# Kernel tuning notes

Measured on AMD Instinct MI355X. Metric: run time of the kernel, lower is better.

## Reference

```python
import jax, jax.numpy as jnp
import numpy as np

B, T, S, E, H, D = 4, 1024, 1024, 1024, 16, 64


def _ln(x, g, b, eps=1e-5):
    m = x.mean(-1, keepdims=True)
    v = ((x - m) ** 2).mean(-1, keepdims=True)
    return (x - m) * jax.lax.rsqrt(v + eps) * g + b


def _mha(xq, xkv, mask4, Wq, Wk, Wv, Wo, bo):
    # Wq/Wk/Wv: [H, E, D] (stacked per-head bias-free linears)
    q = jnp.einsum('bte,hed->bhtd', xq, Wq)
    k = jnp.einsum('bse,hed->bhsd', xkv, Wk)
    v = jnp.einsum('bse,hed->bhsd', xkv, Wv)
    # NOTE: original scales by C**-0.5 with C = n_embd, not head_size
    wei = jnp.einsum('bhtd,bhsd->bhts', q, k) * (float(E) ** -0.5)
    wei = jnp.where(mask4 == 0, jnp.float32(-1e9), wei)
    wei = jax.nn.softmax(wei, axis=-1)
    o = jnp.einsum('bhts,bhsd->bhtd', wei, v)  # [B,H,T,D]
    b_, h_, t_, d_ = o.shape
    o = o.transpose(0, 2, 1, 3).reshape(b_, t_, h_ * d_)
    return o @ Wo + bo


def setup_inputs() -> dict:
    key = jax.random.key(0)
    ks = jax.random.split(key, 24)
    sd = 0.02
    inp = {
        'x': jax.random.normal(ks[0], (B, T, E), jnp.float32),
        'x_m': jnp.ones((B, 1, T), jnp.int32),
        'ca': jax.random.normal(ks[1], (B, S, E), jnp.float32),
        'ca_m': jnp.ones((B, 1, S), jnp.int32),
        'Wq_s': jax.random.normal(ks[2], (H, E, D), jnp.float32) * sd,
        'Wk_s': jax.random.normal(ks[3], (H, E, D), jnp.float32) * sd,
        'Wv_s': jax.random.normal(ks[4], (H, E, D), jnp.float32) * sd,
        'Wo_s': jax.random.normal(ks[5], (E, E), jnp.float32) * sd,
        'bo_s': jnp.zeros((E,), jnp.float32),
        'Wq_c': jax.random.normal(ks[6], (H, E, D), jnp.float32) * sd,
        'Wk_c': jax.random.normal(ks[7], (H, E, D), jnp.float32) * sd,
        'Wv_c': jax.random.normal(ks[8], (H, E, D), jnp.float32) * sd,
        'Wo_c': jax.random.normal(ks[9], (E, E), jnp.float32) * sd,
        'bo_c': jnp.zeros((E,), jnp.float32),
        'ln1_g': jnp.ones((E,), jnp.float32), 'ln1_b': jnp.zeros((E,), jnp.float32),
        'ln2_g': jnp.ones((E,), jnp.float32), 'ln2_b': jnp.zeros((E,), jnp.float32),
        'ln3_g': jnp.ones((E,), jnp.float32), 'ln3_b': jnp.zeros((E,), jnp.float32),
        'W1': jax.random.normal(ks[10], (E, 4 * E), jnp.float32) * sd,
        'b1': jnp.zeros((4 * E,), jnp.float32),
        'W2': jax.random.normal(ks[11], (4 * E, E), jnp.float32) * sd,
        'b2': jnp.zeros((E,), jnp.float32),
    }
    return inp


def reference(x, x_m, ca, ca_m, Wq_s, Wk_s, Wv_s, Wo_s, bo_s,
              Wq_c, Wk_c, Wv_c, Wo_c, bo_c,
              ln1_g, ln1_b, ln2_g, ln2_b, ln3_g, ln3_b,
              W1, b1, W2, b2):
    tril = jnp.tril(jnp.ones((T, T), jnp.int32))
    # self-attn mask: x_m [B,1,T] & tril [T,T] -> [B,1,T,T] (broadcast over heads)
    self_mask = x_m[:, :, None, :] * tril          # [B,1,T,T]
    cross_mask = ca_m[:, :, None, :]               # [B,1,1,S]
    x = x + _mha(_ln(x, ln1_g, ln1_b), _ln(x, ln1_g, ln1_b) if False else _ln(x, ln1_g, ln1_b), self_mask, Wq_s, Wk_s, Wv_s, Wo_s, bo_s)
    x = x + _mha(_ln(x, ln2_g, ln2_b), ca, cross_mask, Wq_c, Wk_c, Wv_c, Wo_c, bo_c)
    h = _ln(x, ln3_g, ln3_b)
    x = x + (jax.nn.relu(h @ W1 + b1) @ W2 + b2)
    return x
```

## Files before the change

kernel.cpp:

```cpp
#include <hip/hip_runtime.h>
#include <hip/hip_bf16.h>
#include <cstdint>
#include <cstddef>

typedef __attribute__((ext_vector_type(8))) short  s8v;
typedef __attribute__((ext_vector_type(4))) short  s4v;
typedef __attribute__((ext_vector_type(8))) __bf16 b8v;
typedef __attribute__((ext_vector_type(4))) float  f32x4;
typedef __attribute__((ext_vector_type(4))) unsigned u32x4;

__device__ __forceinline__ short f2bf(float f){
  unsigned u = __builtin_bit_cast(unsigned, f);
  unsigned r = (u + 0x7fffu + ((u >> 16) & 1u)) >> 16;
  return (short)(unsigned short)r;
}

__device__ __forceinline__ f32x4 mfma16(s8v a, s8v b, f32x4 c){
  return __builtin_amdgcn_mfma_f32_16x16x32_bf16(
      __builtin_bit_cast(b8v, a), __builtin_bit_cast(b8v, b), c, 0, 0, 0);
}

__device__ __forceinline__ unsigned cvtpk(float a, float b){
  unsigned w;
  asm("v_cvt_pk_bf16_f32 %0, %1, %2" : "=v"(w) : "v"(a), "v"(b));
  return w;
}

__global__ __launch_bounds__(256)
void ln_k(const float* __restrict__ x, const float* __restrict__ g,
          const float* __restrict__ b, short* __restrict__ out)
{
  const int row = blockIdx.x, tid = threadIdx.x;
  const float4 v = ((const float4*)(x + (size_t)row*1024))[tid];
  float s  = v.x+v.y+v.z+v.w;
  float s2 = v.x*v.x+v.y*v.y+v.z*v.z+v.w*v.w;
  #pragma unroll
  for (int off=32; off; off>>=1){ s += __shfl_down(s, off); s2 += __shfl_down(s2, off); }
  __shared__ float red[8];
  const int wave = tid>>6, lane = tid&63;
  if (lane==0){ red[wave]=s; red[4+wave]=s2; }
  __syncthreads();
  s  = red[0]+red[1]+red[2]+red[3];
  s2 = red[4]+red[5]+red[6]+red[7];
  const float mean = s*(1.f/1024.f);
  const float rstd = rsqrtf(s2*(1.f/1024.f) - mean*mean + 1e-5f);
  const float4 gv = ((const float4*)g)[tid];
  const float4 bv = ((const float4*)b)[tid];
  s4v o;
  o[0] = f2bf((v.x-mean)*rstd*gv.x + bv.x);
  o[1] = f2bf((v.y-mean)*rstd*gv.y + bv.y);
  o[2] = f2bf((v.z-mean)*rstd*gv.z + bv.z);
  o[3] = f2bf((v.w-mean)*rstd*gv.w + bv.w);
  *(s4v*)(out + (size_t)row*1024 + tid*4) = o;
}

__global__ __launch_bounds__(256)
void cast_k(const float* __restrict__ in, short* __restrict__ out)
{
  const int i = blockIdx.x*256 + threadIdx.x;
  const float4 v = ((const float4*)in)[i];
  s4v o; o[0]=f2bf(v.x); o[1]=f2bf(v.y); o[2]=f2bf(v.z); o[3]=f2bf(v.w);
  ((s4v*)out)[i] = o;
}

__global__ __launch_bounds__(256)
void tcast_k(const float* __restrict__ in, short* __restrict__ out, int E2, int D2)
{
  __shared__ float t[32][33];
  const int h  = blockIdx.z;
  const int e0 = blockIdx.x*32, d0 = blockIdx.y*32;
  const int tx = threadIdx.x & 31, ty = threadIdx.x >> 5;
  const float* ip = in + (size_t)h*E2*D2;
  #pragma unroll
  for (int r = ty; r < 32; r += 8)
    t[r][tx] = ip[(size_t)(e0+r)*D2 + d0 + tx];
  __syncthreads();
  short* op = out + (size_t)h*D2*E2;
  #pragma unroll
  for (int r = ty; r < 32; r += 8)
    op[(size_t)(d0+r)*E2 + e0 + tx] = f2bf(t[tx][r]);
}

__global__ __launch_bounds__(256)
void vtrans_k(const short* __restrict__ V, int ldv, short* __restrict__ Vt, int S, int H)
{
  __shared__ short t[32][34];
  const int bh = blockIdx.z;
  const int b = bh / H, h = bh % H;
  const int s0 = blockIdx.x*32, d0 = blockIdx.y*32;
  const int tx = threadIdx.x & 31, ty = threadIdx.x >> 5;
  const short* ip = V + (size_t)b*S*ldv + h*64;
  #pragma unroll
  for (int r = ty; r < 32; r += 8)
    t[r][tx] = ip[(size_t)(s0+r)*ldv + d0 + tx];
  __syncthreads();
  short* op = Vt + ((size_t)bh*64 + d0)*S + s0;
  #pragma unroll
  for (int r = ty; r < 32; r += 8)
    op[(size_t)r*S + tx] = t[tx][r];
}

template<int BN, int BIAS, int RELU, int RESID, int WF32>
__global__ __launch_bounds__(256, 2)
void gemm_bt(const short* __restrict__ A, const short* __restrict__ Bt,
             const float* __restrict__ bias, const float* __restrict__ resid,
             short* __restrict__ Cb, float* __restrict__ Cf,
             int M, int N, int K)
{
  __shared__ short lds[3][128*32 + BN*32];
  const int nwg = gridDim.x * gridDim.y;
  int id = blockIdx.y * gridDim.x + blockIdx.x;
  id = (id & 7) * (nwg >> 3) + (id >> 3);
  const int bx = id % gridDim.x, by = id / gridDim.x;
  const int m0 = by*128, n0 = bx*BN;

  const int tid  = threadIdx.x;
  const int wave = tid>>6, lane = tid&63;
  const int lo = lane&15, hi = lane>>4;
  const int wm = wave>>1, wn = wave&1;

  constexpr int NJ = BN/32;
  constexpr int BC = BN>>6;
  f32x4 acc[4][NJ] = {};
  const int NK = K >> 5;

  auto stage = [&](int buf, int kt){
    const short* Ag = A  + (size_t)m0*K + kt*32;
    const short* Bg = Bt + (size_t)n0*K + kt*32;
    #pragma unroll
    for (int c=0;c<2;c++){
      const int q = (wave*2+c)*64 + lane;
      const int r = q>>2, cc = q&3;
      __builtin_amdgcn_global_load_lds(
        (const __attribute__((address_space(1))) void*)(Ag + (size_t)r*K + cc*8),
        (__attribute__((address_space(3))) void*)(&lds[buf][(wave*2+c)*512]),
        16, 0, 0);
    }
    #pragma unroll
    for (int c=0;c<BC;c++){
      const int q = (wave*BC+c)*64 + lane;
      const int r = q>>2, cc = q&3;
      __builtin_amdgcn_global_load_lds(
        (const __attribute__((address_space(1))) void*)(Bg + (size_t)r*K + cc*8),
        (__attribute__((address_space(3))) void*)(&lds[buf][4096 + (wave*BC+c)*512]),
        16, 0, 0);
    }
  };

  stage(0, 0);
  if (NK > 1) stage(1, 1);

  for (int kt=0; kt<NK; kt++){
    if (kt+1 < NK){
      if constexpr (BN==128) asm volatile("s_waitcnt vmcnt(4)" ::: "memory");
      else                   asm volatile("s_waitcnt vmcnt(3)" ::: "memory");
    } else {
      asm volatile("s_waitcnt vmcnt(0)" ::: "memory");
    }
    __builtin_amdgcn_s_barrier();
    __builtin_amdgcn_sched_barrier(0);
    if (kt+2 < NK) stage((kt+2)%3, kt+2);

    const short* la = &lds[kt%3][0];
    const short* lb = &lds[kt%3][4096];
    s8v af[4], bfr[NJ];
    #pragma unroll
    for (int i=0;i<4;i++)
      af[i] = *(const s8v*)(la + (wm*64 + i*16 + lo)*32 + hi*8);
    #pragma unroll
    for (int j=0;j<NJ;j++)
      bfr[j] = *(const s8v*)(lb + (wn*(BN/2) + j*16 + lo)*32 + hi*8);
    #pragma unroll
    for (int i=0;i<4;i++)
      #pragma unroll
      for (int j=0;j<NJ;j++)
        acc[i][j] = mfma16(af[i], bfr[j], acc[i][j]);
  }

  #pragma unroll
  for (int i=0;i<4;i++){
    const int row = m0 + wm*64 + i*16 + hi*4;
    #pragma unroll
    for (int j=0;j<NJ;j++){
      const int col = n0 + wn*(BN/2) + j*16 + lo;
      const float bv = BIAS ? bias[col] : 0.0f;
      #pragma unroll
      for (int r=0;r<4;r++){
        float v = acc[i][j][r] + bv;
        if (RELU) v = fmaxf(v, 0.0f);
        const size_t idx = (size_t)(row + r)*N + col;
        if (RESID) v += resid[idx];
        if (WF32) Cf[idx] = v; else Cb[idx] = f2bf(v);
      }
    }
  }
}

template<int CAUSAL>
__global__ __launch_bounds__(256, 4)
void attn_k(const short* __restrict__ Q, int ldq,
            const short* __restrict__ K, int ldk,
            const short* __restrict__ Vt, int ldvt,
            const int* __restrict__ msk,
            short* __restrict__ O, int ldo,
            int H, int Tq, int Sk)
{
  __shared__ short kls[2][4096];
  __shared__ short vls[2][4096];
  const int bh = blockIdx.x;
  const int b = bh / H, h = bh % H;
  const int tid = threadIdx.x;
  const int wave = tid>>6, lane = tid&63;
  const int lo = lane&15, hi = lane>>4;
  const int t0 = blockIdx.y*64 + wave*16;

  const short* Qb  = Q + (size_t)(b*Tq)*ldq + h*64;
  const short* Kb  = K + (size_t)(b*Sk)*ldk + h*64;
  const short* Vtb = Vt + (size_t)bh*64*ldvt;
  const int*   mb  = msk + (size_t)b*Sk;

  const short* qp = Qb + (size_t)(t0+lo)*ldq + hi*8;
  const s8v qa0 = *(const s8v*)(qp);
  const s8v qa1 = *(const s8v*)(qp + 32);

  float mrow = -INFINITY, lrow = 0.f;
  f32x4 oacc[4] = {};
  const int trow = t0 + lo;
  const int nblk = CAUSAL ? (blockIdx.y + 1) : (Sk>>6);
  const float sc2 = 0.03125f * 1.44269504088896f;
  const int x8 = lo & 7;

  auto stage = [&](int buf, int it){
    const int s0 = it*64;
    #pragma unroll
    for (int rd=0; rd<2; rd++){
      const int q = rd*256 + tid;
      const int r = q>>3, c = q&7;
      const int cs = (c ^ (r&7))*8;
      __builtin_amdgcn_global_load_lds(
        (const __attribute__((address_space(1))) void*)(Kb + (size_t)(s0+r)*ldk + cs),
        (__attribute__((address_space(3))) void*)(&kls[buf][(rd*256 + wave*64)*8]),
        16, 0, 0);
      __builtin_amdgcn_global_load_lds(
        (const __attribute__((address_space(1))) void*)(Vtb + (size_t)r*ldvt + s0 + cs),
        (__attribute__((address_space(3))) void*)(&vls[buf][(rd*256 + wave*64)*8]),
        16, 0, 0);
    }
  };

  stage(0, 0);
  int cur = 0;
  for (int it=0; it<nblk; it++){
    __syncthreads();
    if (it+1 < nblk) stage(cur^1, it+1);
    const int s0 = it*64;

    int ka[4][4];
    #pragma unroll
    for (int g=0; g<4; g++){
      const int4 kv = ((const int4*)mb)[(s0>>2) + g*4 + hi];
      ka[g][0]=kv.x; ka[g][1]=kv.y; ka[g][2]=kv.z; ka[g][3]=kv.w;
    }

    const short* kl = kls[cur];
    s8v kf[4][2];
    #pragma unroll
    for (int g=0; g<4; g++){
      const int rb = (g*16 + lo)*64;
      kf[g][0] = *(const s8v*)(kl + rb + ((hi     ^ x8)*8));
      kf[g][1] = *(const s8v*)(kl + rb + (((4+hi) ^ x8)*8));
    }

    f32x4 sg[4] = {};
    __builtin_amdgcn_s_setprio(1);
    #pragma unroll
    for (int g=0; g<4; g++){
      sg[g] = mfma16(kf[g][0], qa0, sg[g]);
      sg[g] = mfma16(kf[g][1], qa1, sg[g]);
    }
    __builtin_amdgcn_s_setprio(0);

    const bool lastblk = CAUSAL && (it == nblk-1);
    float p[4][4];
    #pragma unroll
    for (int g=0; g<4; g++)
      #pragma unroll
      for (int r=0; r<4; r++){
        const int sidx = s0 + g*16 + 4*hi + r;
        const bool ok = ka[g][r] && (!lastblk || sidx <= trow);
        p[g][r] = ok ? sg[g][r]*sc2 : -1.5e9f;
      }

    float bmax;
    {
      float m0_ = fmaxf(fmaxf(p[0][0],p[0][1]), fmaxf(p[0][2],p[0][3]));
      float m1_ = fmaxf(fmaxf(p[1][0],p[1][1]), fmaxf(p[1][2],p[1][3]));
      float m2_ = fmaxf(fmaxf(p[2][0],p[2][1]), fmaxf(p[2][2],p[2][3]));
      float m3_ = fmaxf(fmaxf(p[3][0],p[3][1]), fmaxf(p[3][2],p[3][3]));
      bmax = fmaxf(fmaxf(m0_,m1_), fmaxf(m2_,m3_));
    }
    bmax = fmaxf(bmax, __shfl_xor(bmax, 16));
    bmax = fmaxf(bmax, __shfl_xor(bmax, 32));

    const float mn  = fmaxf(mrow, bmax);
    const float fac = exp2f(mrow - mn);
    mrow = mn;
    #pragma unroll
    for (int g=0; g<4; g++)
      #pragma unroll
      for (int r=0; r<4; r++)
        p[g][r] = exp2f(p[g][r] - mn);

    float bsum;
    {
      float s0_ = (p[0][0]+p[0][1]) + (p[0][2]+p[0][3]);
      float s1_ = (p[1][0]+p[1][1]) + (p[1][2]+p[1][3]);
      float s2_ = (p[2][0]+p[2][1]) + (p[2][2]+p[2][3]);
      float s3_ = (p[3][0]+p[3][1]) + (p[3][2]+p[3][3]);
      bsum = (s0_+s1_) + (s2_+s3_);
    }
    bsum += __shfl_xor(bsum, 16);
    bsum += __shfl_xor(bsum, 32);
    lrow = lrow*fac + bsum;
    #pragma unroll
    for (int f=0; f<4; f++)
      #pragma unroll
      for (int r=0; r<4; r++)
        oacc[f][r] *= fac;

    u32x4 pw0, pw1;
    pw0[0] = cvtpk(p[0][0], p[0][1]);
    pw0[1] = cvtpk(p[0][2], p[0][3]);
    pw0[2] = cvtpk(p[1][0], p[1][1]);
    pw0[3] = cvtpk(p[1][2], p[1][3]);
    pw1[0] = cvtpk(p[2][0], p[2][1]);
    pw1[1] = cvtpk(p[2][2], p[2][3]);
    pw1[2] = cvtpk(p[3][0], p[3][1]);
    pw1[3] = cvtpk(p[3][2], p[3][3]);
    const s8v pb0 = __builtin_bit_cast(s8v, pw0);
    const s8v pb1 = __builtin_bit_cast(s8v, pw1);

    const short* vl = vls[cur];
    __builtin_amdgcn_s_setprio(1);
    #pragma unroll
    for (int f=0; f<4; f++){
      const int rb = (f*16 + lo)*64;
      const int h2 = hi>>1, o2 = (hi&1)*4;
      const s4v a0 = *(const s4v*)(vl + rb + (((h2  ) ^ x8)*8) + o2);
      const s4v a1 = *(const s4v*)(vl + rb + (((2+h2) ^ x8)*8) + o2);
      const s4v a2 = *(const s4v*)(vl + rb + (((4+h2) ^ x8)*8) + o2);
      const s4v a3 = *(const s4v*)(vl + rb + (((6+h2) ^ x8)*8) + o2);
      const s8v av0 = __builtin_shufflevector(a0, a1, 0,1,2,3,4,5,6,7);
      const s8v av1 = __builtin_shufflevector(a2, a3, 0,1,2,3,4,5,6,7);
      oacc[f] = mfma16(av0, pb0, oacc[f]);
      oacc[f] = mfma16(av1, pb1, oacc[f]);
    }
    __builtin_amdgcn_s_setprio(0);
    cur ^= 1;
  }

  const float inv = 1.0f / lrow;
  short* Ob = O + (size_t)(b*Tq)*ldo + h*64 + (size_t)(t0+lo)*ldo + 4*hi;
  #pragma unroll
  for (int f=0; f<4; f++){
    s4v o;
    #pragma unroll
    for (int r=0; r<4; r++) o[r] = f2bf(oacc[f][r]*inv);
    *(s4v*)(Ob + f*16) = o;
  }
}

extern "C" void kernel_launch(void* const* d_in, const int* in_sizes, int n_in,
                              void* d_out, int out_size, void* d_ws, size_t ws_size,
                              hipStream_t stream)
{
  (void)in_sizes; (void)n_in; (void)out_size; (void)ws_size;
  const float* x    = (const float*)d_in[0];
  const int*   xm   = (const int*)  d_in[1];
  const float* ca   = (const float*)d_in[2];
  const int*   cam  = (const int*)  d_in[3];
  const float* Wq_s = (const float*)d_in[4];
  const float* Wk_s = (const float*)d_in[5];
  const float* Wv_s = (const float*)d_in[6];
  const float* Wo_s = (const float*)d_in[7];
  const float* bo_s = (const float*)d_in[8];
  const float* Wq_c = (const float*)d_in[9];
  const float* Wk_c = (const float*)d_in[10];
  const float* Wv_c = (const float*)d_in[11];
  const float* Wo_c = (const float*)d_in[12];
  const float* bo_c = (const float*)d_in[13];
  const float* ln1g = (const float*)d_in[14];
  const float* ln1b = (const float*)d_in[15];
  const float* ln2g = (const float*)d_in[16];
  const float* ln2b = (const float*)d_in[17];
  const float* ln3g = (const float*)d_in[18];
  const float* ln3b = (const float*)d_in[19];
  const float* W1   = (const float*)d_in[20];
  const float* b1   = (const float*)d_in[21];
  const float* W2   = (const float*)d_in[22];
  const float* b2   = (const float*)d_in[23];
  float* out = (float*)d_out;

  char* ws = (char*)d_ws;
  size_t off = 0;
  auto alloc = [&](size_t bytes)->void*{
    void* p = ws + off; off += (bytes + 255) & ~(size_t)255; return p; };

  short* w_qkv_s = (short*)alloc((size_t)3072*1024*2);
  short* w_o_s   = (short*)alloc((size_t)1024*1024*2);
  short* w_q_c   = (short*)alloc((size_t)1024*1024*2);
  short* w_kv_c  = (short*)alloc((size_t)2048*1024*2);
  short* w_o_c   = (short*)alloc((size_t)1024*1024*2);
  short* w_1     = (short*)alloc((size_t)4096*1024*2);
  short* w_2     = (short*)alloc((size_t)1024*4096*2);
  short* xn      = (short*)alloc((size_t)4096*1024*2);
  short* cab     = (short*)alloc((size_t)4096*1024*2);
  short* qkv     = (short*)alloc((size_t)4096*3072*2);
  short* attno   = (short*)alloc((size_t)4096*1024*2);
  float* xres    = (float*)alloc((size_t)4096*1024*4);
  short* hffn    = (short*)alloc((size_t)4096*4096*2);
  short* kvbuf   = qkv + (size_t)4096*1024;
  short* vt_s    = hffn;
  short* vt_c    = hffn + (size_t)4*1024*1024;

  tcast_k<<<dim3(32,  2,16),256,0,stream>>>(Wq_s, w_qkv_s,           1024,   64);
  tcast_k<<<dim3(32,  2,16),256,0,stream>>>(Wk_s, w_qkv_s+1024*1024, 1024,   64);
  tcast_k<<<dim3(32,  2,16),256,0,stream>>>(Wv_s, w_qkv_s+2048*1024, 1024,   64);
  tcast_k<<<dim3(32, 32, 1),256,0,stream>>>(Wo_s, w_o_s,             1024, 1024);
  tcast_k<<<dim3(32,  2,16),256,0,stream>>>(Wq_c, w_q_c,             1024,   64);
  tcast_k<<<dim3(32,  2,16),256,0,stream>>>(Wk_c, w_kv_c,            1024,   64);
  tcast_k<<<dim3(32,  2,16),256,0,stream>>>(Wv_c, w_kv_c+1024*1024,  1024,   64);
  tcast_k<<<dim3(32, 32, 1),256,0,stream>>>(Wo_c, w_o_c,             1024, 1024);
  tcast_k<<<dim3(32,128, 1),256,0,stream>>>(W1,   w_1,               1024, 4096);
  tcast_k<<<dim3(128,32, 1),256,0,stream>>>(W2,   w_2,               4096, 1024);
  cast_k<<<4096,256,0,stream>>>(ca, cab);

  ln_k<<<4096,256,0,stream>>>(x, ln1g, ln1b, xn);
  gemm_bt<128,0,0,0,0><<<dim3(24,32),256,0,stream>>>(xn, w_qkv_s, nullptr, nullptr,
                                                     qkv, nullptr, 4096, 3072, 1024);
  vtrans_k<<<dim3(32,2,64),256,0,stream>>>(qkv+2048, 3072, vt_s, 1024, 16);
  attn_k<1><<<dim3(64,16),256,0,stream>>>(qkv, 3072, qkv+1024, 3072, vt_s, 1024,
                                          xm, attno, 1024, 16, 1024, 1024);
  gemm_bt<64,1,0,1,1><<<dim3(16,32),256,0,stream>>>(attno, w_o_s, bo_s, x,
                                                    nullptr, xres, 4096, 1024, 1024);

  ln_k<<<4096,256,0,stream>>>(xres, ln2g, ln2b, xn);
  gemm_bt<64,0,0,0,0><<<dim3(16,32),256,0,stream>>>(xn, w_q_c, nullptr, nullptr,
                                                    qkv, nullptr, 4096, 1024, 1024);
  gemm_bt<64,0,0,0,0><<<dim3(32,32),256,0,stream>>>(cab, w_kv_c, nullptr, nullptr,
                                                    kvbuf, nullptr, 4096, 2048, 1024);
  vtrans_k<<<dim3(32,2,64),256,0,stream>>>(kvbuf+1024, 2048, vt_c, 1024, 16);
  attn_k<0><<<dim3(64,16),256,0,stream>>>(qkv, 1024, kvbuf, 2048, vt_c, 1024,
                                          cam, attno, 1024, 16, 1024, 1024);
  gemm_bt<64,1,0,1,1><<<dim3(16,32),256,0,stream>>>(attno, w_o_c, bo_c, xres,
                                                    nullptr, xres, 4096, 1024, 1024);

  ln_k<<<4096,256,0,stream>>>(xres, ln3g, ln3b, xn);
  gemm_bt<128,1,1,0,0><<<dim3(32,32),256,0,stream>>>(xn, w_1, b1, nullptr,
                                                     hffn, nullptr, 4096, 4096, 1024);
  gemm_bt<64,1,0,1,1><<<dim3(16,32),256,0,stream>>>(hffn, w_2, b2, xres,
                                                    nullptr, out, 4096, 1024, 4096);
}
```

Measured before the change: 394.3 us.

## Add 256x128 eight-wave GEMM with swizzled LDS and split-K FFN down-projection

Adds a new 512-thread GEMM kernel with 256x128 output tiles, 64-wide K steps, XOR-swizzled LDS staging through direct global-to-LDS loads, a three-buffer prefetch pipeline and raised wave priority around the MFMA blocks. It replaces the self-attention QKV, cross-attention KV and FFN up-projection GEMMs. The FFN down-projection is split into two K-halves writing fp32 partial sums, and a separate reduction kernel adds them together with bias and residual. The intent is more data reuse per tile and more blocks for the down-projection. The cost is extra partial-sum memory traffic, one more kernel launch, and occupancy limited to one block per CU.

```diff
diff --git a/kernel.cpp b/kernel.cpp
--- a/kernel.cpp
+++ b/kernel.cpp
@@ -100,6 +100,22 @@
     op[(size_t)r*S + tx] = t[tx][r];
 }
 
+__global__ __launch_bounds__(256)
+void red2_k(const float* __restrict__ pa, const float* __restrict__ pb,
+            const float* __restrict__ bias, const float* __restrict__ resid,
+            float* __restrict__ out, int N)
+{
+  const int i = blockIdx.x*256 + threadIdx.x;
+  const float4 va = ((const float4*)pa)[i];
+  const float4 vb = ((const float4*)pb)[i];
+  const float4 vr = ((const float4*)resid)[i];
+  const float4 bv = ((const float4*)bias)[i & (N/4 - 1)];
+  float4 o;
+  o.x = va.x+vb.x+bv.x+vr.x; o.y = va.y+vb.y+bv.y+vr.y;
+  o.z = va.z+vb.z+bv.z+vr.z; o.w = va.w+vb.w+bv.w+vr.w;
+  ((float4*)out)[i] = o;
+}
+
 template<int BN, int BIAS, int RELU, int RESID, int WF32>
 __global__ __launch_bounds__(256, 2)
 void gemm_bt(const short* __restrict__ A, const short* __restrict__ Bt,
@@ -187,6 +203,117 @@
       #pragma unroll
       for (int r=0;r<4;r++){
         float v = acc[i][j][r] + bv;
+        if (RELU) v = fmaxf(v, 0.0f);
+        const size_t idx = (size_t)(row + r)*N + col;
+        if (RESID) v += resid[idx];
+        if (WF32) Cf[idx] = v; else Cb[idx] = f2bf(v);
+      }
+    }
+  }
+}
+
+template<int BIAS, int RELU, int RESID, int WF32>
+__global__ __launch_bounds__(512, 1)
+void gemm8(const short* __restrict__ A, int lda,
+           const short* __restrict__ Bt, int ldb,
+           const float* __restrict__ bias, const float* __restrict__ resid,
+           short* __restrict__ Cb, float* __restrict__ Cf,
+           int M, int N, int K)
+{
+  __shared__ short lds[3][24576];
+  const int nwg = gridDim.x * gridDim.y;
+  int id = blockIdx.y * gridDim.x + blockIdx.x;
+  id = (id & 7) * (nwg >> 3) + (id >> 3);
+  const int bx = id % gridDim.x, by = id / gridDim.x;
+  const int m0 = by*256, n0 = bx*128;
+
+  const int tid = threadIdx.x;
+  const int lane = tid&63, wave = tid>>6;
+  const int lo = lane&15, hi = lane>>4;
+  const int wr = wave>>2, wc = wave&3;
+  const int x8 = lo&7;
+
+  f32x4 acc[8][2] = {};
+  const int NT = K >> 6;
+
+  auto stageA = [&](int buf, int kt, int part){
+    const short* Ag = A + (size_t)m0*lda + kt*64;
+    #pragma unroll
+    for (int j=0;j<2;j++){
+      const int q = (part*2+j)*512 + tid;
+      const int r = q>>3, c = q&7;
+      __builtin_amdgcn_global_load_lds(
+        (const __attribute__((address_space(1))) void*)(Ag + (size_t)r*lda + ((c^(r&7))*8)),
+        (__attribute__((address_space(3))) void*)(&lds[buf][q*8]), 16, 0, 0);
+    }
+  };
+  auto stageB = [&](int buf, int kt, int part){
+    const short* Bg = Bt + (size_t)n0*ldb + kt*64;
+    const int q = part*512 + tid;
+    const int r = q>>3, c = q&7;
+    __builtin_amdgcn_global_load_lds(
+      (const __attribute__((address_space(1))) void*)(Bg + (size_t)r*ldb + ((c^(r&7))*8)),
+      (__attribute__((address_space(3))) void*)(&lds[buf][16384 + q*8]), 16, 0, 0);
+  };
+
+  stageA(0,0,0); stageA(0,0,1); stageB(0,0,0); stageB(0,0,1);
+  if (NT>1){ stageA(1,1,0); stageA(1,1,1); stageB(1,1,0); stageB(1,1,1); }
+  asm volatile("s_waitcnt vmcnt(6)" ::: "memory");
+  __builtin_amdgcn_s_barrier();
+
+  for (int t=0; t<NT; t++){
+    const short* la = &lds[t%3][0];
+    const short* lb = &lds[t%3][16384];
+    const int nb = (t+2)%3;
+    const bool pf = (t+2 < NT);
+    #pragma unroll
+    for (int q=0; q<4; q++){
+      const int mh = q>>1, ks = q&1;
+      s8v af[4], bf2[2];
+      #pragma unroll
+      for (int i=0;i<4;i++){
+        const int row = wr*128 + (mh*4+i)*16 + lo;
+        af[i] = *(const s8v*)(la + row*64 + (((ks*4+hi)^x8)*8));
+      }
+      #pragma unroll
+      for (int j=0;j<2;j++){
+        const int row = wc*32 + j*16 + lo;
+        bf2[j] = *(const s8v*)(lb + row*64 + (((ks*4+hi)^x8)*8));
+      }
+      if (pf){
+        if      (q==0) stageA(nb, t+2, 0);
+        else if (q==1) stageA(nb, t+2, 1);
+        else if (q==2) stageB(nb, t+2, 0);
+        else           stageB(nb, t+2, 1);
+      }
+      __builtin_amdgcn_s_barrier();
+      asm volatile("s_waitcnt lgkmcnt(0)" ::: "memory");
+      __builtin_amdgcn_sched_barrier(0);
+      __builtin_amdgcn_s_setprio(1);
+      #pragma unroll
+      for (int i=0;i<4;i++)
+        #pragma unroll
+        for (int j=0;j<2;j++)
+          acc[mh*4+i][j] = mfma16(af[i], bf2[j], acc[mh*4+i][j]);
+      __builtin_amdgcn_s_setprio(0);
+      if (q==3 && t+1 < NT){
+        if (pf) asm volatile("s_waitcnt vmcnt(6)" ::: "memory");
+        else    asm volatile("s_waitcnt vmcnt(0)" ::: "memory");
+      }
+      __builtin_amdgcn_s_barrier();
+    }
+  }
+
+  #pragma unroll
+  for (int I=0;I<8;I++){
+    const int row = m0 + wr*128 + I*16 + hi*4;
+    #pragma unroll
+    for (int j=0;j<2;j++){
+      const int col = n0 + wc*32 + j*16 + lo;
+      const float bv = BIAS ? bias[col] : 0.0f;
+      #pragma unroll
+      for (int r=0;r<4;r++){
+        float v = acc[I][j][r] + bv;
         if (RELU) v = fmaxf(v, 0.0f);
         const size_t idx = (size_t)(row + r)*N + col;
         if (RESID) v += resid[idx];
@@ -419,6 +546,8 @@
   short* attno   = (short*)alloc((size_t)4096*1024*2);
   float* xres    = (float*)alloc((size_t)4096*1024*4);
   short* hffn    = (short*)alloc((size_t)4096*4096*2);
+  float* pA      = (float*)alloc((size_t)4096*1024*4);
+  float* pB      = (float*)alloc((size_t)4096*1024*4);
   short* kvbuf   = qkv + (size_t)4096*1024;
   short* vt_s    = hffn;
   short* vt_c    = hffn + (size_t)4*1024*1024;
@@ -436,8 +565,9 @@
   cast_k<<<4096,256,0,stream>>>(ca, cab);
 
   ln_k<<<4096,256,0,stream>>>(x, ln1g, ln1b, xn);
-  gemm_bt<128,0,0,0,0><<<dim3(24,32),256,0,stream>>>(xn, w_qkv_s, nullptr, nullptr,
-                                                     qkv, nullptr, 4096, 3072, 1024);
+  gemm8<0,0,0,0><<<dim3(24,16),512,0,stream>>>(xn, 1024, w_qkv_s, 1024,
+                                               nullptr, nullptr, qkv, nullptr,
+                                               4096, 3072, 1024);
   vtrans_k<<<dim3(32,2,64),256,0,stream>>>(qkv+2048, 3072, vt_s, 1024, 16);
   attn_k<1><<<dim3(64,16),256,0,stream>>>(qkv, 3072, qkv+1024, 3072, vt_s, 1024,
                                           xm, attno, 1024, 16, 1024, 1024);
@@ -447,8 +577,9 @@
   ln_k<<<4096,256,0,stream>>>(xres, ln2g, ln2b, xn);
   gemm_bt<64,0,0,0,0><<<dim3(16,32),256,0,stream>>>(xn, w_q_c, nullptr, nullptr,
                                                     qkv, nullptr, 4096, 1024, 1024);
-  gemm_bt<64,0,0,0,0><<<dim3(32,32),256,0,stream>>>(cab, w_kv_c, nullptr, nullptr,
-                                                    kvbuf, nullptr, 4096, 2048, 1024);
+  gemm8<0,0,0,0><<<dim3(16,16),512,0,stream>>>(cab, 1024, w_kv_c, 1024,
+                                               nullptr, nullptr, kvbuf, nullptr,
+                                               4096, 2048, 1024);
   vtrans_k<<<dim3(32,2,64),256,0,stream>>>(kvbuf+1024, 2048, vt_c, 1024, 16);
   attn_k<0><<<dim3(64,16),256,0,stream>>>(qkv, 1024, kvbuf, 2048, vt_c, 1024,
                                           cam, attno, 1024, 16, 1024, 1024);
@@ -456,8 +587,14 @@
                                                     nullptr, xres, 4096, 1024, 1024);
 
   ln_k<<<4096,256,0,stream>>>(xres, ln3g, ln3b, xn);
-  gemm_bt<128,1,1,0,0><<<dim3(32,32),256,0,stream>>>(xn, w_1, b1, nullptr,
-                                                     hffn, nullptr, 4096, 4096, 1024);
-  gemm_bt<64,1,0,1,1><<<dim3(16,32),256,0,stream>>>(hffn, w_2, b2, xres,
-                                                    nullptr, out, 4096, 1024, 4096);
-}
+  gemm8<1,1,0,0><<<dim3(32,16),512,0,stream>>>(xn, 1024, w_1, 1024,
+                                               b1, nullptr, hffn, nullptr,
+                                               4096, 4096, 1024);
+  gemm8<0,0,0,1><<<dim3(8,16),512,0,stream>>>(hffn,      4096, w_2,      4096,
+                                              nullptr, nullptr, nullptr, pA,
+                                              4096, 1024, 2048);
+  gemm8<0,0,0,1><<<dim3(8,16),512,0,stream>>>(hffn+2048, 4096, w_2+2048, 4096,
+                                              nullptr, nullptr, nullptr, pB,
+                                              4096, 1024, 2048);
+  red2_k<<<4096,256,0,stream>>>(pA, pB, b2, xres, out, 1024);
+}
```

Measured after the change: 434.3 us. 1.1x slower.
